# Kernel tuning notes

Hardware: AMD Instinct MI355X
Metric: run time of the kernel (lower is better)

The kernel has to match this reference:

```python
import jax, jax.numpy as jnp
import numpy as np

N, LDIMS, HID, HID2 = 1024, 256, 128, 64


def setup_inputs() -> dict:
    key = jax.random.key(0)
    ks = jax.random.split(key, 8)
    return {
        "x": jax.random.normal(ks[0], (N, 2, LDIMS), dtype=jnp.float32),
        "W_foh": jax.random.normal(ks[1], (2 * LDIMS, HID), dtype=jnp.float32) * 0.05,
        "W_fom": jax.random.normal(ks[2], (2 * LDIMS, HID), dtype=jnp.float32) * 0.05,
        "cat_bias": jax.random.normal(ks[3], (2 * HID,), dtype=jnp.float32) * 0.05,
        "W_hid2": jax.random.normal(ks[4], (2 * HID, HID2), dtype=jnp.float32) * 0.05,
        "hid2_bias": jax.random.normal(ks[5], (HID2,), dtype=jnp.float32) * 0.05,
        "W_out": jax.random.normal(ks[6], (HID2, 1), dtype=jnp.float32) * 0.05,
        "out_bias": jax.random.normal(ks[7], (1,), dtype=jnp.float32) * 0.05,
    }


def reference(x, W_foh, W_fom, cat_bias, W_hid2, hid2_bias, W_out, out_bias):
    n = x.shape[0]
    h = W_foh.shape[1]
    xf = x.reshape(n, -1)                      # concat(lstms_0, lstms_1) -> [n, 2*ldims]
    headfov = xf @ W_foh                       # [n, h]
    modfov = xf @ W_fom                        # [n, h]
    # Original: tanh(concat(headfov_i, modfov_j) + catBias) @ W_hid2.
    # tanh is elementwise, and concat @ W_hid2 splits exactly into top/bottom blocks,
    # so we precompute per-node terms instead of materializing [n, n, 2h].
    th = jnp.tanh(headfov + cat_bias[:h]) @ W_hid2[:h]    # [n, hid2]
    tm = jnp.tanh(modfov + cat_bias[h:]) @ W_hid2[h:]     # [n, hid2]
    pre = th[:, None, :] + tm[None, :, :] + hid2_bias     # [n, n, hid2]
    h2 = jnp.tanh(pre)
    scores = jnp.einsum('ijd,do->ijo', h2, W_out)[..., 0] + out_bias[0]  # [n, n]
    return scores
```

## Files before the change

### kernel.cpp

```cpp
#include <hip/hip_runtime.h>
#include <hip/hip_bf16.h>
#include <stdint.h>

typedef __attribute__((ext_vector_type(8))) short bf16x8;
typedef __attribute__((ext_vector_type(4))) float f32x4;

#define NN 1024
#define KD 512
#define NC 256
#define H2 64

#define OFF_A    0
#define OFF_WT   1048576
#define OFF_WHB  1310720
#define OFF_G    1343488
#define OFF_PT   1867776
#define OFF_QT   2129920

#define TANH_SCALE 2.8853900817779268f

static __device__ __forceinline__ ushort f2bf(float f) {
    uint32_t u = __builtin_bit_cast(uint32_t, f);
    uint32_t r = (u + 0x7fffu + ((u >> 16) & 1u)) >> 16;
    return (ushort)r;
}

__global__ __launch_bounds__(256) void k0_pack(const float* __restrict__ x,
                                               const float* __restrict__ W_foh,
                                               const float* __restrict__ W_fom,
                                               const float* __restrict__ W_hid2,
                                               ushort* __restrict__ A,
                                               ushort* __restrict__ Wt,
                                               ushort* __restrict__ Whb) {
    int tid = blockIdx.x * 256 + threadIdx.x;
    if (tid < 131072) {
        float4 v = ((const float4*)x)[tid];
        ushort4 o;
        o.x = f2bf(v.x); o.y = f2bf(v.y); o.z = f2bf(v.z); o.w = f2bf(v.w);
        ((ushort4*)A)[tid] = o;
    } else if (tid < 262144) {
        int t2 = tid - 131072;
        int c = t2 & 255, k = t2 >> 8;
        float v = (c < 128) ? W_foh[k * 128 + c] : W_fom[k * 128 + c - 128];
        Wt[c * 512 + k] = f2bf(v);
    } else if (tid < 278528) {
        int t3 = tid - 262144;
        int d = t3 & 63, c = t3 >> 6;
        Whb[d * 256 + c] = f2bf(W_hid2[c * 64 + d]);
    }
}

__global__ __launch_bounds__(256) void k1_gemm1(const ushort* __restrict__ A,
                                                const ushort* __restrict__ Wt,
                                                const float* __restrict__ cat_bias,
                                                ushort* __restrict__ g) {
    __shared__ float red[4 * 64 * 4];
    int lane = threadIdx.x & 63;
    int wave = threadIdx.x >> 6;
    int b = blockIdx.x;
    int ntile = b & 15;
    int mtile = b >> 4;
    int l15 = lane & 15;
    int kofs = wave * 128 + (lane >> 4) * 8;
    const ushort* Ar = A + (mtile * 16 + l15) * 512 + kofs;
    const ushort* Br = Wt + (ntile * 16 + l15) * 512 + kofs;
    f32x4 acc = {0.f, 0.f, 0.f, 0.f};
#pragma unroll
    for (int s = 0; s < 4; ++s) {
        bf16x8 a = *(const bf16x8*)(Ar + s * 32);
        bf16x8 bb = *(const bf16x8*)(Br + s * 32);
        acc = __builtin_amdgcn_mfma_f32_16x16x32_bf16(a, bb, acc, 0, 0, 0);
    }
    *(f32x4*)(&red[(wave * 64 + lane) * 4]) = acc;
    __syncthreads();
    if (wave == 0) {
        f32x4 s0 = *(const f32x4*)(&red[(0 * 64 + lane) * 4]);
        f32x4 s1 = *(const f32x4*)(&red[(1 * 64 + lane) * 4]);
        f32x4 s2 = *(const f32x4*)(&red[(2 * 64 + lane) * 4]);
        f32x4 s3 = *(const f32x4*)(&red[(3 * 64 + lane) * 4]);
        int col = ntile * 16 + l15;
        float cb = cat_bias[col];
#pragma unroll
        for (int r = 0; r < 4; ++r) {
            int row = mtile * 16 + (lane >> 4) * 4 + r;
            float xv = s0[r] + s1[r] + s2[r] + s3[r] + cb;
            float e = exp2f(xv * TANH_SCALE);
            float t = 1.0f - 2.0f * __builtin_amdgcn_rcpf(e + 1.0f);
            g[row * 256 + col] = f2bf(t);
        }
    }
}

__global__ __launch_bounds__(256) void k2_gemm2(const ushort* __restrict__ g,
                                                const ushort* __restrict__ Whb,
                                                const float* __restrict__ hid2_bias,
                                                float* __restrict__ Pt,
                                                float* __restrict__ Qt) {
    int lane = threadIdx.x & 63;
    int wv = blockIdx.x * 4 + (threadIdx.x >> 6);
    int mtile = wv & 63;
    int dtile = (wv >> 6) & 3;
    int half = wv >> 8;
    int cbase = half * 128;
    int l15 = lane & 15;
    int kofs = (lane >> 4) * 8;
    const ushort* Ar = g + (mtile * 16 + l15) * 256 + cbase + kofs;
    const ushort* Br = Whb + (dtile * 16 + l15) * 256 + cbase + kofs;
    f32x4 acc = {0.f, 0.f, 0.f, 0.f};
#pragma unroll
    for (int s = 0; s < 4; ++s) {
        bf16x8 a = *(const bf16x8*)(Ar + s * 32);
        bf16x8 bb = *(const bf16x8*)(Br + s * 32);
        acc = __builtin_amdgcn_mfma_f32_16x16x32_bf16(a, bb, acc, 0, 0, 0);
    }
    int dcol = dtile * 16 + l15;
    float* out = half ? Qt : Pt;
    float badd = half ? 0.0f : hid2_bias[dcol];
#pragma unroll
    for (int r = 0; r < 4; ++r) {
        int i = mtile * 16 + (lane >> 4) * 4 + r;
        out[dcol * 1024 + i] = (acc[r] + badd) * TANH_SCALE;
    }
}

__global__ __launch_bounds__(256) void k3_scores(const float* __restrict__ Pt,
                                                 const float* __restrict__ Qt,
                                                 const float* __restrict__ W_out,
                                                 const float* __restrict__ out_bias,
                                                 float* __restrict__ out) {
    __shared__ float Pl[64][68];
    __shared__ float Ql[64][36];
    __shared__ float wl[64];
    int t = threadIdx.x;
    int b = blockIdx.x;
    int i0 = (b >> 5) * 64;
    int j0 = (b & 31) * 32;
    {
        int rowd = t >> 2;
        int cch = (t & 3) * 16;
        const float4* ps = (const float4*)(Pt + rowd * 1024 + i0 + cch);
#pragma unroll
        for (int u = 0; u < 4; ++u) *(float4*)(&Pl[rowd][cch + u * 4]) = ps[u];
    }
    {
        int rowd = t >> 2;
        int cch = (t & 3) * 8;
        const float4* qs = (const float4*)(Qt + rowd * 1024 + j0 + cch);
        *(float4*)(&Ql[rowd][cch]) = qs[0];
        *(float4*)(&Ql[rowd][cch + 4]) = qs[1];
    }
    if (t < 64) wl[t] = -2.0f * W_out[t];
    float base = out_bias[0];
#pragma unroll
    for (int d = 0; d < 64; ++d) base += W_out[d];
    __syncthreads();

    int il = (t & 15) * 4;
    int jl = (t >> 4) * 2;
    float acc[4][2] = {};
#pragma unroll 8
    for (int d = 0; d < 64; ++d) {
        f32x4 p = *(const f32x4*)(&Pl[d][il]);
        float q0 = Ql[d][jl], q1 = Ql[d][jl + 1];
        float w = wl[d];
#pragma unroll
        for (int a = 0; a < 4; ++a) {
            float e0 = exp2f(p[a] + q0);
            float r0 = __builtin_amdgcn_rcpf(e0 + 1.0f);
            acc[a][0] = fmaf(w, r0, acc[a][0]);
            float e1 = exp2f(p[a] + q1);
            float r1 = __builtin_amdgcn_rcpf(e1 + 1.0f);
            acc[a][1] = fmaf(w, r1, acc[a][1]);
        }
    }
#pragma unroll
    for (int a = 0; a < 4; ++a) {
        float2 v;
        v.x = base + acc[a][0];
        v.y = base + acc[a][1];
        *(float2*)(&out[(i0 + il + a) * 1024 + j0 + jl]) = v;
    }
}

extern "C" void kernel_launch(void* const* d_in, const int* in_sizes, int n_in,
                              void* d_out, int out_size, void* d_ws, size_t ws_size,
                              hipStream_t stream) {
    const float* x        = (const float*)d_in[0];
    const float* W_foh    = (const float*)d_in[1];
    const float* W_fom    = (const float*)d_in[2];
    const float* cat_bias = (const float*)d_in[3];
    const float* W_hid2   = (const float*)d_in[4];
    const float* hid2_bias= (const float*)d_in[5];
    const float* W_out    = (const float*)d_in[6];
    const float* out_bias = (const float*)d_in[7];

    char* ws = (char*)d_ws;
    ushort* A   = (ushort*)(ws + OFF_A);
    ushort* Wt  = (ushort*)(ws + OFF_WT);
    ushort* Whb = (ushort*)(ws + OFF_WHB);
    ushort* g   = (ushort*)(ws + OFF_G);
    float*  Pt  = (float*)(ws + OFF_PT);
    float*  Qt  = (float*)(ws + OFF_QT);

    k0_pack<<<1088, 256, 0, stream>>>(x, W_foh, W_fom, W_hid2, A, Wt, Whb);
    k1_gemm1<<<1024, 256, 0, stream>>>(A, Wt, cat_bias, g);
    k2_gemm2<<<128, 256, 0, stream>>>(g, Whb, hid2_bias, Pt, Qt);
    k3_scores<<<512, 256, 0, stream>>>(Pt, Qt, W_out, out_bias, (float*)d_out);
}
```

Measured before the change: 103.9 us.

## Fuse both projection GEMMs and tanh into one kernel, convert x inline

Merges the first GEMM (with tanh), the second GEMM and the x-to-bf16 conversion into a single kernel. Each block handles 16 rows and one half, keeps the tanh activations in shared memory and goes straight into the W_hid2 product. This removes a kernel launch, the A and g workspace round trips, and the split-K shared reduction. The tradeoff is only 128 blocks, each running a longer K loop of 16 steps, which lowers parallelism for the first GEMM.

```diff
diff --git a/kernel.cpp b/kernel.cpp
--- a/kernel.cpp
+++ b/kernel.cpp
@@ -10,12 +10,10 @@
 #define NC 256
 #define H2 64
 
-#define OFF_A    0
-#define OFF_WT   1048576
-#define OFF_WHB  1310720
-#define OFF_G    1343488
-#define OFF_PT   1867776
-#define OFF_QT   2129920
+#define OFF_WT   0
+#define OFF_WHB  262144
+#define OFF_PT   294912
+#define OFF_QT   557056
 
 #define TANH_SCALE 2.8853900817779268f
 
@@ -25,101 +23,94 @@
     return (ushort)r;
 }
 
-__global__ __launch_bounds__(256) void k0_pack(const float* __restrict__ x,
-                                               const float* __restrict__ W_foh,
+__global__ __launch_bounds__(256) void k0_pack(const float* __restrict__ W_foh,
                                                const float* __restrict__ W_fom,
                                                const float* __restrict__ W_hid2,
-                                               ushort* __restrict__ A,
                                                ushort* __restrict__ Wt,
                                                ushort* __restrict__ Whb) {
     int tid = blockIdx.x * 256 + threadIdx.x;
     if (tid < 131072) {
-        float4 v = ((const float4*)x)[tid];
-        ushort4 o;
-        o.x = f2bf(v.x); o.y = f2bf(v.y); o.z = f2bf(v.z); o.w = f2bf(v.w);
-        ((ushort4*)A)[tid] = o;
-    } else if (tid < 262144) {
-        int t2 = tid - 131072;
-        int c = t2 & 255, k = t2 >> 8;
+        int c = tid & 255, k = tid >> 8;
         float v = (c < 128) ? W_foh[k * 128 + c] : W_fom[k * 128 + c - 128];
         Wt[c * 512 + k] = f2bf(v);
-    } else if (tid < 278528) {
-        int t3 = tid - 262144;
+    } else if (tid < 147456) {
+        int t3 = tid - 131072;
         int d = t3 & 63, c = t3 >> 6;
         Whb[d * 256 + c] = f2bf(W_hid2[c * 64 + d]);
     }
 }
 
-__global__ __launch_bounds__(256) void k1_gemm1(const ushort* __restrict__ A,
+__global__ __launch_bounds__(256) void kA_fused(const float* __restrict__ x,
                                                 const ushort* __restrict__ Wt,
+                                                const ushort* __restrict__ Whb,
                                                 const float* __restrict__ cat_bias,
-                                                ushort* __restrict__ g) {
-    __shared__ float red[4 * 64 * 4];
+                                                const float* __restrict__ hid2_bias,
+                                                float* __restrict__ Pt,
+                                                float* __restrict__ Qt) {
+    __shared__ ushort hl[16 * 136];
     int lane = threadIdx.x & 63;
     int wave = threadIdx.x >> 6;
     int b = blockIdx.x;
-    int ntile = b & 15;
-    int mtile = b >> 4;
+    int half = b & 1;
+    int itile = b >> 1;
+    int i0 = itile * 16;
     int l15 = lane & 15;
-    int kofs = wave * 128 + (lane >> 4) * 8;
-    const ushort* Ar = A + (mtile * 16 + l15) * 512 + kofs;
-    const ushort* Br = Wt + (ntile * 16 + l15) * 512 + kofs;
+    int kq = lane >> 4;
+    int kofs = kq * 8;
+
+    const float* xr = x + (i0 + l15) * 512 + kofs;
+    int nt0 = wave * 2;
+    const ushort* B0 = Wt + (half * 128 + nt0 * 16 + l15) * 512 + kofs;
+    const ushort* B1 = B0 + 16 * 512;
+    f32x4 acc0 = {0.f, 0.f, 0.f, 0.f};
+    f32x4 acc1 = {0.f, 0.f, 0.f, 0.f};
+#pragma unroll
+    for (int s = 0; s < 16; ++s) {
+        float4 xa = *(const float4*)(xr + s * 32);
+        float4 xb = *(const float4*)(xr + s * 32 + 4);
+        bf16x8 a;
+        a[0] = (short)f2bf(xa.x); a[1] = (short)f2bf(xa.y);
+        a[2] = (short)f2bf(xa.z); a[3] = (short)f2bf(xa.w);
+        a[4] = (short)f2bf(xb.x); a[5] = (short)f2bf(xb.y);
+        a[6] = (short)f2bf(xb.z); a[7] = (short)f2bf(xb.w);
+        bf16x8 b0 = *(const bf16x8*)(B0 + s * 32);
+        bf16x8 b1 = *(const bf16x8*)(B1 + s * 32);
+        acc0 = __builtin_amdgcn_mfma_f32_16x16x32_bf16(a, b0, acc0, 0, 0, 0);
+        acc1 = __builtin_amdgcn_mfma_f32_16x16x32_bf16(a, b1, acc1, 0, 0, 0);
+    }
+    {
+        int c0 = nt0 * 16 + l15;
+        float cb0 = cat_bias[half * 128 + c0];
+        float cb1 = cat_bias[half * 128 + c0 + 16];
+#pragma unroll
+        for (int r = 0; r < 4; ++r) {
+            int row = kq * 4 + r;
+            float v0 = acc0[r] + cb0;
+            float v1 = acc1[r] + cb1;
+            float t0 = 1.0f - 2.0f * __builtin_amdgcn_rcpf(exp2f(v0 * TANH_SCALE) + 1.0f);
+            float t1 = 1.0f - 2.0f * __builtin_amdgcn_rcpf(exp2f(v1 * TANH_SCALE) + 1.0f);
+            hl[row * 136 + c0] = f2bf(t0);
+            hl[row * 136 + c0 + 16] = f2bf(t1);
+        }
+    }
+    __syncthreads();
+
+    int dt = wave;
+    const ushort* B2 = Whb + (dt * 16 + l15) * 256 + half * 128 + kofs;
     f32x4 acc = {0.f, 0.f, 0.f, 0.f};
 #pragma unroll
     for (int s = 0; s < 4; ++s) {
-        bf16x8 a = *(const bf16x8*)(Ar + s * 32);
-        bf16x8 bb = *(const bf16x8*)(Br + s * 32);
+        bf16x8 a = *(const bf16x8*)(&hl[l15 * 136 + kofs + s * 32]);
+        bf16x8 bb = *(const bf16x8*)(B2 + s * 32);
         acc = __builtin_amdgcn_mfma_f32_16x16x32_bf16(a, bb, acc, 0, 0, 0);
     }
-    *(f32x4*)(&red[(wave * 64 + lane) * 4]) = acc;
-    __syncthreads();
-    if (wave == 0) {
-        f32x4 s0 = *(const f32x4*)(&red[(0 * 64 + lane) * 4]);
-        f32x4 s1 = *(const f32x4*)(&red[(1 * 64 + lane) * 4]);
-        f32x4 s2 = *(const f32x4*)(&red[(2 * 64 + lane) * 4]);
-        f32x4 s3 = *(const f32x4*)(&red[(3 * 64 + lane) * 4]);
-        int col = ntile * 16 + l15;
-        float cb = cat_bias[col];
-#pragma unroll
-        for (int r = 0; r < 4; ++r) {
-            int row = mtile * 16 + (lane >> 4) * 4 + r;
-            float xv = s0[r] + s1[r] + s2[r] + s3[r] + cb;
-            float e = exp2f(xv * TANH_SCALE);
-            float t = 1.0f - 2.0f * __builtin_amdgcn_rcpf(e + 1.0f);
-            g[row * 256 + col] = f2bf(t);
-        }
-    }
-}
-
-__global__ __launch_bounds__(256) void k2_gemm2(const ushort* __restrict__ g,
-                                                const ushort* __restrict__ Whb,
-                                                const float* __restrict__ hid2_bias,
-                                                float* __restrict__ Pt,
-                                                float* __restrict__ Qt) {
-    int lane = threadIdx.x & 63;
-    int wv = blockIdx.x * 4 + (threadIdx.x >> 6);
-    int mtile = wv & 63;
-    int dtile = (wv >> 6) & 3;
-    int half = wv >> 8;
-    int cbase = half * 128;
-    int l15 = lane & 15;
-    int kofs = (lane >> 4) * 8;
-    const ushort* Ar = g + (mtile * 16 + l15) * 256 + cbase + kofs;
-    const ushort* Br = Whb + (dtile * 16 + l15) * 256 + cbase + kofs;
-    f32x4 acc = {0.f, 0.f, 0.f, 0.f};
-#pragma unroll
-    for (int s = 0; s < 4; ++s) {
-        bf16x8 a = *(const bf16x8*)(Ar + s * 32);
-        bf16x8 bb = *(const bf16x8*)(Br + s * 32);
-        acc = __builtin_amdgcn_mfma_f32_16x16x32_bf16(a, bb, acc, 0, 0, 0);
-    }
-    int dcol = dtile * 16 + l15;
+    int d = dt * 16 + l15;
     float* out = half ? Qt : Pt;
-    float badd = half ? 0.0f : hid2_bias[dcol];
+    float badd = half ? 0.0f : hid2_bias[d];
 #pragma unroll
     for (int r = 0; r < 4; ++r) {
-        int i = mtile * 16 + (lane >> 4) * 4 + r;
-        out[dcol * 1024 + i] = (acc[r] + badd) * TANH_SCALE;
+        int i = i0 + kq * 4 + r;
+        out[d * 1024 + i] = (acc[r] + badd) * TANH_SCALE;
     }
 }
 
@@ -195,15 +186,12 @@
     const float* out_bias = (const float*)d_in[7];
 
     char* ws = (char*)d_ws;
-    ushort* A   = (ushort*)(ws + OFF_A);
     ushort* Wt  = (ushort*)(ws + OFF_WT);
     ushort* Whb = (ushort*)(ws + OFF_WHB);
-    ushort* g   = (ushort*)(ws + OFF_G);
     float*  Pt  = (float*)(ws + OFF_PT);
     float*  Qt  = (float*)(ws + OFF_QT);
 
-    k0_pack<<<1088, 256, 0, stream>>>(x, W_foh, W_fom, W_hid2, A, Wt, Whb);
-    k1_gemm1<<<1024, 256, 0, stream>>>(A, Wt, cat_bias, g);
-    k2_gemm2<<<128, 256, 0, stream>>>(g, Whb, hid2_bias, Pt, Qt);
+    k0_pack<<<576, 256, 0, stream>>>(W_foh, W_fom, W_hid2, Wt, Whb);
+    kA_fused<<<128, 256, 0, stream>>>(x, Wt, Whb, cat_bias, hid2_bias, Pt, Qt);
     k3_scores<<<512, 256, 0, stream>>>(Pt, Qt, W_out, out_bias, (float*)d_out);
 }
```

Result: no change. 104.8 us (+0.8%).
